# Performance work log

Measured on AMD Instinct MI355X. Metric: run time of the kernel, lower is better.

The kernel has to match this reference:

```python
import jax, jax.numpy as jnp
import numpy as np

NUM_HEADS = 16
HIDDEN = 1024
HEAD_DIM = HIDDEN // NUM_HEADS
B, S, D = 2, 2048, 1024


def setup_inputs() -> dict:
    key = jax.random.key(0)
    ks = jax.random.split(key, 7)
    scale = 1.0 / np.sqrt(D)
    return {
        "query": jax.random.normal(ks[0], (B, S, D), dtype=jnp.float32),
        "key": jax.random.normal(ks[1], (B, S, D), dtype=jnp.float32),
        "value": jax.random.normal(ks[2], (B, S, D), dtype=jnp.float32),
        "Wk_w": jax.random.normal(ks[3], (HIDDEN, D), dtype=jnp.float32) * scale,
        "Wk_b": jax.random.normal(ks[4], (HIDDEN,), dtype=jnp.float32) * scale,
        "Wv_w": jax.random.normal(ks[5], (HIDDEN, D), dtype=jnp.float32) * scale,
        "Wv_b": jax.random.normal(ks[6], (HIDDEN,), dtype=jnp.float32) * scale,
    }


def reference(query, key, value, Wk_w, Wk_b, Wv_w, Wv_b):
    # NOTE: in the original torch module, self.W_v is assigned twice, so the
    # SAME Linear (Wv) projects both key and value; Wk projects query.
    b, s, _ = query.shape

    def split_heads(x):  # [b,s,hidden] -> [b,h,s,hd]
        return x.reshape(b, s, NUM_HEADS, HEAD_DIM).transpose(0, 2, 1, 3)

    q = split_heads(query @ Wk_w.T + Wk_b)
    k = split_heads(key @ Wv_w.T + Wv_b)
    v = split_heads(value @ Wv_w.T + Wv_b)

    scores = jnp.einsum("bhqd,bhkd->bhqk", q, k) / jnp.sqrt(
        jnp.asarray(HEAD_DIM, dtype=q.dtype))
    probs = jax.nn.softmax(scores, axis=-1)
    out = jnp.einsum("bhqk,bhkd->bhqd", probs, v)
    return out.transpose(0, 2, 1, 3).reshape(b, s, NUM_HEADS * HEAD_DIM)
```

## Files before the change

kernel.cpp:

```cpp
#include <hip/hip_runtime.h>
#include <stdint.h>

typedef unsigned short u16;
typedef uint32_t u32;
typedef __bf16 bf16x8 __attribute__((ext_vector_type(8)));
typedef float f32x4 __attribute__((ext_vector_type(4)));
typedef float f32x16 __attribute__((ext_vector_type(16)));
typedef u16 u16x4 __attribute__((ext_vector_type(4)));
typedef u16 u16x8 __attribute__((ext_vector_type(8)));

#define XQ_OFF 0ul
#define XK_OFF 4194304ul
#define XV_OFF 8388608ul
#define WK_OFF 12582912ul
#define WV_OFF 13631488ul
#define Q_OFF  14680064ul
#define K_OFF  18874368ul
#define V_OFF  23068672ul

#define SCQ 0.18033688011112042f

#if __has_builtin(__builtin_amdgcn_exp2f)
#define EXP2F(x) __builtin_amdgcn_exp2f(x)
#else
#define EXP2F(x) exp2f(x)
#endif

__device__ __forceinline__ u16 f2bf(float f) {
  u32 u = __float_as_uint(f);
  u32 r = (u + 0x7fffu + ((u >> 16) & 1u)) >> 16;
  return (u16)r;
}

__device__ __forceinline__ u32 pk2(float a, float b) {
  typedef __bf16 bf2_t __attribute__((ext_vector_type(2)));
  typedef float f2_t __attribute__((ext_vector_type(2)));
  f2_t v; v[0] = a; v[1] = b;
  bf2_t h = __builtin_convertvector(v, bf2_t);
  union { bf2_t h; u32 u; } cv; cv.h = h; return cv.u;
}

__device__ __forceinline__ void load_lds16(const void* g, void* l) {
  __builtin_amdgcn_global_load_lds(
      (const __attribute__((address_space(1))) u32*)g,
      (__attribute__((address_space(3))) u32*)l, 16, 0, 0);
}

__device__ __forceinline__ u32 swz(u32 L) {
  return L ^ (((L >> 7) & 1u) << 4) ^ (((L >> 10) & 3u) << 5);
}

__global__ __launch_bounds__(256) void cvt_tile_kernel(
    const float* __restrict__ xq, const float* __restrict__ xk,
    const float* __restrict__ xv, const float* __restrict__ wk,
    const float* __restrict__ wv, u16* __restrict__ ws) {
  __shared__ u16 tile[4096];
  const int bid = blockIdx.x;
  const float* src; size_t dstbase; int rt, ktp;
  if (bid < 3072) {
    int m = bid >> 10, loc = bid & 1023;
    src = (m == 0) ? xq : (m == 1) ? xk : xv;
    dstbase = (size_t)m * 4194304ul;
    rt = loc >> 4; ktp = loc & 15;
  } else {
    int r2 = bid - 3072;
    int m = r2 >> 8, loc = r2 & 255;
    src = m ? wv : wk;
    dstbase = WK_OFF + (size_t)m * 1048576ul;
    rt = loc >> 4; ktp = loc & 15;
  }
  const int t = threadIdx.x;
  const int row0 = t >> 4, c = t & 15;
  const int k = c * 4;
  const float* s = src + (size_t)(rt * 64 + row0) * 1024ul + ktp * 64 + k;
#pragma unroll
  for (int i = 0; i < 4; ++i) {
    float4 v = *(const float4*)(s + (size_t)i * 16384ul);
    int row = row0 + i * 16;
    u32* p = (u32*)(tile + ((k >> 5) * 2048 + ((k >> 3) & 3) * 512 + row * 8 + (k & 7)));
    p[0] = pk2(v.x, v.y);
    p[1] = pk2(v.z, v.w);
  }
  __syncthreads();
  u16* dst = ws + dstbase + (size_t)(rt * 32 + ktp * 2) * 2048ul;
#pragma unroll
  for (int so = 0; so < 4096; so += 2048)
    *(u16x8*)(dst + so + t * 8) = *(const u16x8*)(tile + so + t * 8);
}

__global__ __launch_bounds__(256, 2) void proj_kernel(u16* __restrict__ ws,
                                                      const float* __restrict__ bk,
                                                      const float* __restrict__ bv) {
  const int proj = blockIdx.z;
  const int mtile = blockIdx.x;
  const int ntile = blockIdx.y;
  const u16* A = ws + (size_t)proj * 4194304ul;
  const u16* Bw = ws + ((proj == 0) ? WK_OFF : WV_OFF);
  const float* bias = (proj == 0) ? bk : bv;
  u16* outQ = ws + Q_OFF;
  u16* outK = ws + K_OFF;
  u16* outV = ws + V_OFF;

  const int t = threadIdx.x;
  const int w = t >> 6, lane = t & 63;
  const int wm = w >> 1, wn = w & 1;
  const int g = lane >> 4, c = lane & 15;

  __shared__ __align__(16) u16 smem[32768];

  const u16* Ag = A + (size_t)(2 * mtile) * 65536ul;
  const u16* Bg = Bw + (size_t)(2 * ntile) * 65536ul;
  const u32 t8 = (u32)t * 8u;
  const u32 so = swz((u32)t * 16u) >> 1;

  u32 poff[4];
#pragma unroll
  for (int mt = 0; mt < 4; ++mt)
    poff[mt] = swz((u32)((g << 10) | ((mt * 16 + c) << 4))) >> 1;

#define PSTAGE(buf, kt)                                            \
  do {                                                             \
    u16* bb = smem + (buf) * 8192;                                 \
    const size_t ko = (size_t)(kt) * 2048ul + so;                  \
    load_lds16(Ag + ko, bb + t8);                                  \
    load_lds16(Ag + 65536ul + ko, bb + 2048 + t8);                 \
    load_lds16(Bg + ko, bb + 4096 + t8);                           \
    load_lds16(Bg + 65536ul + ko, bb + 6144 + t8);                 \
  } while (0)

#define PFRAGS_MFMA(buf)                                                        \
  do {                                                                          \
    const u16* Ap = smem + (buf) * 8192 + wm * 2048;                            \
    const u16* Bp = smem + (buf) * 8192 + 4096 + wn * 2048;                     \
    bf16x8 af[4], bfv[4];                                                       \
    _Pragma("unroll") for (int mt = 0; mt < 4; ++mt)                            \
        af[mt] = *(const bf16x8*)(Ap + poff[mt]);                               \
    _Pragma("unroll") for (int nt = 0; nt < 4; ++nt)                            \
        bfv[nt] = *(const bf16x8*)(Bp + poff[nt]);                              \
    _Pragma("unroll") for (int mt = 0; mt < 4; ++mt)                            \
        _Pragma("unroll") for (int nt = 0; nt < 4; ++nt)                        \
            acc[mt][nt] = __builtin_amdgcn_mfma_f32_16x16x32_bf16(              \
                af[mt], bfv[nt], acc[mt][nt], 0, 0, 0);                         \
  } while (0)

  f32x4 acc[4][4];
#pragma unroll
  for (int mt = 0; mt < 4; ++mt)
#pragma unroll
    for (int nt = 0; nt < 4; ++nt) acc[mt][nt] = (f32x4){0.f, 0.f, 0.f, 0.f};

  PSTAGE(0, 0);
  PSTAGE(1, 1);
  PSTAGE(2, 2);
  PSTAGE(3, 3);

#pragma unroll 1
  for (int p = 0; p < 15; ++p) {
    asm volatile("s_waitcnt vmcnt(8)\n\ts_barrier" ::: "memory");
    const int b0 = (2 * p) & 3;
    PFRAGS_MFMA(b0);
    PFRAGS_MFMA(b0 + 1);
    __builtin_amdgcn_s_barrier();
    if (p < 14) {
      PSTAGE(b0, 2 * p + 4);
      PSTAGE(b0 + 1, 2 * p + 5);
    }
  }
  asm volatile("s_waitcnt vmcnt(0)\n\ts_barrier" ::: "memory");
  PFRAGS_MFMA(2);
  PFRAGS_MFMA(3);
#undef PSTAGE
#undef PFRAGS_MFMA

  const int m0 = mtile * 128 + wm * 64;
  const int n0 = ntile * 128 + wn * 64;
  if (proj == 2) {
#pragma unroll
    for (int nt = 0; nt < 4; ++nt) {
      const int col = n0 + nt * 16 + c;
      const float bvv = bias[col];
      const int h = col >> 6, d = col & 63;
#pragma unroll
      for (int mt = 0; mt < 4; ++mt) {
        const int mbase = m0 + mt * 16 + g * 4;
        const int b = mbase >> 11;
        const int bh = b * 16 + h;
        const int s = mbase & 2047;
        u16x4 pk;
#pragma unroll
        for (int r = 0; r < 4; ++r) pk[r] = f2bf(acc[mt][nt][r] + bvv);
        size_t idx = (size_t)bh * 131072ul + (size_t)(s >> 6) * 4096ul +
                     (size_t)((s & 63) >> 3) * 512ul + (size_t)d * 8ul + (size_t)(s & 7);
        *(u16x4*)(outV + idx) = pk;
      }
    }
  } else {
    __syncthreads();
    u16* Ew = smem + w * 4096;
#pragma unroll
    for (int nt = 0; nt < 4; ++nt) {
      const int d = nt * 16 + c;
      const float bvv = bias[n0 + nt * 16 + c];
#pragma unroll
      for (int mt = 0; mt < 4; ++mt) {
#pragma unroll
        for (int r = 0; r < 4; ++r) {
          const int srow = mt * 16 + g * 4 + r;
          float y = acc[mt][nt][r] + bvv;
          if (proj == 0) y *= SCQ;
          Ew[(d >> 3) * 512 + srow * 8 + (d & 7)] = f2bf(y);
        }
      }
    }
    __syncthreads();
    const int b = mtile >> 4;
    const int bh = b * 16 + ntile * 2 + wn;
    if (proj == 0) {
      u16* base = outQ + (size_t)bh * 131072ul + (size_t)(mtile & 15) * 8192ul + wm * 512;
#pragma unroll
      for (int i = 0; i < 8; ++i)
        *(u16x8*)(base + i * 1024 + lane * 8) = *(const u16x8*)(Ew + i * 512 + lane * 8);
    } else {
      u16* base = outK + (size_t)bh * 131072ul + (size_t)((mtile & 15) * 2 + wm) * 4096ul;
#pragma unroll
      for (int i = 0; i < 8; ++i)
        *(u16x8*)(base + i * 512 + lane * 8) = *(const u16x8*)(Ew + i * 512 + lane * 8);
    }
  }
}

__global__ __launch_bounds__(512, 4) void attn_kernel(u16* __restrict__ ws,
                                                      float* __restrict__ out) {
  const int bh = blockIdx.x, qtile = blockIdx.y;
  const int b = bh >> 4, h = bh & 15;
  const int t = threadIdx.x, w = t >> 6, lane = t & 63;
  const int c32 = lane & 31, g2 = lane >> 5;
  const int hf = w >> 2;
  const int wi = w & 3;

  __shared__ __align__(16) u16 smemA[32768];

  const u16* Qg = ws + Q_OFF + (size_t)bh * 131072ul + (size_t)qtile * 8192ul;

  const int hfs = t >> 8, tt = t & 255;
  const u16* KgS = ws + K_OFF + (size_t)bh * 131072ul + (size_t)hfs * 65536ul;
  const u16* VgS = ws + V_OFF + (size_t)bh * 131072ul + (size_t)hfs * 65536ul;
  u16* kb0 = smemA + hfs * 2 * 4096;
  u16* vb0 = smemA + 16384 + hfs * 2 * 4096;

  const u16* Kb0 = smemA + hf * 2 * 4096;
  const u16* Vb0 = smemA + 16384 + hf * 2 * 4096;

  bf16x8 qf[4];
#pragma unroll
  for (int ks = 0; ks < 4; ++ks)
    qf[ks] = *(const bf16x8*)(Qg + (size_t)(ks * 2 + g2) * 1024ul +
                              (size_t)(wi * 32 + c32) * 8ul);

  f32x16 O0, O1, Lacc;
#pragma unroll
  for (int i = 0; i < 16; ++i) { O0[i] = 0.f; O1[i] = 0.f; Lacc[i] = 0.f; }

#define STAGE_KV(buf, jj)                                          \
  do {                                                             \
    const u16* Kj = KgS + (size_t)(jj) * 4096ul;                   \
    const u16* Vj = VgS + (size_t)(jj) * 4096ul;                   \
    u16* kb = kb0 + (buf) * 4096;                                  \
    u16* vb = vb0 + (buf) * 4096;                                  \
    load_lds16(Kj + (size_t)tt * 8ul, kb + tt * 8);                \
    load_lds16(Kj + 2048ul + (size_t)tt * 8ul, kb + 2048 + tt * 8);\
    load_lds16(Vj + (size_t)tt * 8ul, vb + tt * 8);                \
    load_lds16(Vj + 2048ul + (size_t)tt * 8ul, vb + 2048 + tt * 8);\
  } while (0)

  STAGE_KV(0, 0);

#pragma unroll 1
  for (int j = 0; j < 16; ++j) {
    asm volatile("s_waitcnt vmcnt(0)\n\ts_barrier" ::: "memory");
    if (j < 15) STAGE_KV((j + 1) & 1, j + 1);
    const u16* Kb = Kb0 + (j & 1) * 4096;
    const u16* Vb = Vb0 + (j & 1) * 4096;

    f32x16 S0, S1;
#pragma unroll
    for (int i = 0; i < 16; ++i) { S0[i] = 0.f; S1[i] = 0.f; }
    __builtin_amdgcn_s_setprio(1);
#pragma unroll
    for (int ks = 0; ks < 4; ++ks) {
      bf16x8 kf0 = *(const bf16x8*)(Kb + (ks * 2 + g2) * 512 + c32 * 8);
      bf16x8 kf1 = *(const bf16x8*)(Kb + (ks * 2 + g2) * 512 + (32 + c32) * 8);
      S0 = __builtin_amdgcn_mfma_f32_32x32x16_bf16(kf0, qf[ks], S0, 0, 0, 0);
      S1 = __builtin_amdgcn_mfma_f32_32x32x16_bf16(kf1, qf[ks], S1, 0, 0, 0);
    }
    __builtin_amdgcn_s_setprio(0);

#pragma unroll
    for (int i = 0; i < 16; ++i) { S0[i] = EXP2F(S0[i]); S1[i] = EXP2F(S1[i]); }
    Lacc += S0;
    Lacc += S1;

    u32 pa[4][4];
#pragma unroll
    for (int half = 0; half < 2; ++half) {
      const f32x16& Sx = half ? S1 : S0;
#pragma unroll
      for (int sub = 0; sub < 2; ++sub) {
        const int rb = sub * 8;
        u32 q0 = pk2(Sx[rb + 0], Sx[rb + 1]);
        u32 q1 = pk2(Sx[rb + 2], Sx[rb + 3]);
        u32 q2 = pk2(Sx[rb + 4], Sx[rb + 5]);
        u32 q3 = pk2(Sx[rb + 6], Sx[rb + 7]);
        asm volatile("v_permlane32_swap_b32 %0, %1" : "+v"(q0), "+v"(q2));
        asm volatile("v_permlane32_swap_b32 %0, %1" : "+v"(q1), "+v"(q3));
        const int kstep = half * 2 + sub;
        pa[kstep][0] = q0; pa[kstep][1] = q1; pa[kstep][2] = q2; pa[kstep][3] = q3;
      }
    }

    __builtin_amdgcn_s_setprio(1);
#pragma unroll
    for (int kstep = 0; kstep < 4; ++kstep) {
      union { u32 u[4]; bf16x8 b; } pcv;
#pragma unroll
      for (int i = 0; i < 4; ++i) pcv.u[i] = pa[kstep][i];
      bf16x8 vf0 = *(const bf16x8*)(Vb + (kstep * 2 + g2) * 512 + c32 * 8);
      bf16x8 vf1 = *(const bf16x8*)(Vb + (kstep * 2 + g2) * 512 + (32 + c32) * 8);
      O0 = __builtin_amdgcn_mfma_f32_32x32x16_bf16(pcv.b, vf0, O0, 0, 0, 0);
      O1 = __builtin_amdgcn_mfma_f32_32x32x16_bf16(pcv.b, vf1, O1, 0, 0, 0);
    }
    __builtin_amdgcn_s_setprio(0);
  }
#undef STAGE_KV

  float lp = 0.f;
#pragma unroll
  for (int i = 0; i < 16; ++i) lp += Lacc[i];
  float lA = lp, lB = lp;
  asm volatile("v_permlane32_swap_b32 %0, %1" : "+v"(lA), "+v"(lB));
  float Ltot = lA + lB;

  asm volatile("s_waitcnt lgkmcnt(0)" ::: "memory");
  __syncthreads();
  float* exch = (float*)smemA;
  float* ex = exch + (size_t)(wi * 64 + lane) * 33ul;
  if (hf == 1) {
#pragma unroll
    for (int i = 0; i < 16; ++i) { ex[i] = O0[i]; ex[16 + i] = O1[i]; }
    ex[32] = Ltot;
  }
  __syncthreads();
  if (hf == 0) {
    const float Ltc = Ltot + ex[32];
    const int q0 = qtile * 128 + wi * 32;
    float* outb = out + (size_t)(b * 2048 + q0) * 1024ul + h * 64 + c32;
#pragma unroll
    for (int r = 0; r < 16; ++r) {
      const int qr = (r & 3) + 8 * (r >> 2) + 4 * g2;
      int lv = __builtin_amdgcn_ds_bpermute(qr << 2, __float_as_int(Ltc));
      const float inv = 1.0f / __int_as_float(lv);
      float* rp = outb + (size_t)qr * 1024ul;
      rp[0] = (O0[r] + ex[r]) * inv;
      rp[32] = (O1[r] + ex[16 + r]) * inv;
    }
  }
}

extern "C" void kernel_launch(void* const* d_in, const int* in_sizes, int n_in,
                              void* d_out, int out_size, void* d_ws, size_t ws_size,
                              hipStream_t stream) {
  const float* q = (const float*)d_in[0];
  const float* k = (const float*)d_in[1];
  const float* v = (const float*)d_in[2];
  const float* wk = (const float*)d_in[3];
  const float* bk = (const float*)d_in[4];
  const float* wv = (const float*)d_in[5];
  const float* bv = (const float*)d_in[6];
  u16* ws = (u16*)d_ws;
  float* out = (float*)d_out;

  cvt_tile_kernel<<<3584, 256, 0, stream>>>(q, k, v, wk, wv, ws);
  proj_kernel<<<dim3(32, 8, 3), 256, 0, stream>>>(ws, bk, bv);
  attn_kernel<<<dim3(32, 16), 512, 0, stream>>>(ws, out);
}
```

Measured before the change: 174.6 us.

## Fuse fp32-to-bf16 conversion into projection GEMM, dropping separate convert kernel

New measurement: 197.0 us. 1.13x slower.

```diff
diff --git a/kernel.cpp b/kernel.cpp
--- a/kernel.cpp
+++ b/kernel.cpp
@@ -9,11 +9,6 @@
 typedef u16 u16x4 __attribute__((ext_vector_type(4)));
 typedef u16 u16x8 __attribute__((ext_vector_type(8)));
 
-#define XQ_OFF 0ul
-#define XK_OFF 4194304ul
-#define XV_OFF 8388608ul
-#define WK_OFF 12582912ul
-#define WV_OFF 13631488ul
 #define Q_OFF  14680064ul
 #define K_OFF  18874368ul
 #define V_OFF  23068672ul
@@ -46,56 +41,16 @@
       (__attribute__((address_space(3))) u32*)l, 16, 0, 0);
 }
 
-__device__ __forceinline__ u32 swz(u32 L) {
-  return L ^ (((L >> 7) & 1u) << 4) ^ (((L >> 10) & 3u) << 5);
-}
-
-__global__ __launch_bounds__(256) void cvt_tile_kernel(
+__global__ __launch_bounds__(256, 2) void proj_kernel(
     const float* __restrict__ xq, const float* __restrict__ xk,
     const float* __restrict__ xv, const float* __restrict__ wk,
-    const float* __restrict__ wv, u16* __restrict__ ws) {
-  __shared__ u16 tile[4096];
-  const int bid = blockIdx.x;
-  const float* src; size_t dstbase; int rt, ktp;
-  if (bid < 3072) {
-    int m = bid >> 10, loc = bid & 1023;
-    src = (m == 0) ? xq : (m == 1) ? xk : xv;
-    dstbase = (size_t)m * 4194304ul;
-    rt = loc >> 4; ktp = loc & 15;
-  } else {
-    int r2 = bid - 3072;
-    int m = r2 >> 8, loc = r2 & 255;
-    src = m ? wv : wk;
-    dstbase = WK_OFF + (size_t)m * 1048576ul;
-    rt = loc >> 4; ktp = loc & 15;
-  }
-  const int t = threadIdx.x;
-  const int row0 = t >> 4, c = t & 15;
-  const int k = c * 4;
-  const float* s = src + (size_t)(rt * 64 + row0) * 1024ul + ktp * 64 + k;
-#pragma unroll
-  for (int i = 0; i < 4; ++i) {
-    float4 v = *(const float4*)(s + (size_t)i * 16384ul);
-    int row = row0 + i * 16;
-    u32* p = (u32*)(tile + ((k >> 5) * 2048 + ((k >> 3) & 3) * 512 + row * 8 + (k & 7)));
-    p[0] = pk2(v.x, v.y);
-    p[1] = pk2(v.z, v.w);
-  }
-  __syncthreads();
-  u16* dst = ws + dstbase + (size_t)(rt * 32 + ktp * 2) * 2048ul;
-#pragma unroll
-  for (int so = 0; so < 4096; so += 2048)
-    *(u16x8*)(dst + so + t * 8) = *(const u16x8*)(tile + so + t * 8);
-}
-
-__global__ __launch_bounds__(256, 2) void proj_kernel(u16* __restrict__ ws,
-                                                      const float* __restrict__ bk,
-                                                      const float* __restrict__ bv) {
+    const float* __restrict__ wv, const float* __restrict__ bk,
+    const float* __restrict__ bv, u16* __restrict__ ws) {
   const int proj = blockIdx.z;
   const int mtile = blockIdx.x;
   const int ntile = blockIdx.y;
-  const u16* A = ws + (size_t)proj * 4194304ul;
-  const u16* Bw = ws + ((proj == 0) ? WK_OFF : WV_OFF);
+  const float* xa = (proj == 0) ? xq : (proj == 1) ? xk : xv;
+  const float* wsrc = (proj == 0) ? wk : wv;
   const float* bias = (proj == 0) ? bk : bv;
   u16* outQ = ws + Q_OFF;
   u16* outK = ws + K_OFF;
@@ -106,71 +61,72 @@
   const int wm = w >> 1, wn = w & 1;
   const int g = lane >> 4, c = lane & 15;
 
-  __shared__ __align__(16) u16 smem[32768];
-
-  const u16* Ag = A + (size_t)(2 * mtile) * 65536ul;
-  const u16* Bg = Bw + (size_t)(2 * ntile) * 65536ul;
-  const u32 t8 = (u32)t * 8u;
-  const u32 so = swz((u32)t * 16u) >> 1;
-
-  u32 poff[4];
+  __shared__ __align__(16) float smemf[16384];
+
+  const int srow = t >> 3;
+  const int lchunk = (t & 7) ^ (srow & 7);
+  const float* As0 = xa + (size_t)(mtile * 128 + srow) * 1024ul + lchunk * 4;
+  const float* Bs0 = wsrc + (size_t)(ntile * 128 + srow) * 1024ul + lchunk * 4;
+
+#define PSTAGE(buf, kt)                                                      \
+  do {                                                                       \
+    float* ab = smemf + (buf) * 8192 + t * 4;                                \
+    float* bb = smemf + (buf) * 8192 + 4096 + t * 4;                         \
+    const float* as = As0 + (size_t)(kt) * 32ul;                             \
+    const float* bs = Bs0 + (size_t)(kt) * 32ul;                             \
+    load_lds16(as, ab);                                                      \
+    load_lds16(as + 32768, ab + 1024);                                       \
+    load_lds16(as + 65536, ab + 2048);                                       \
+    load_lds16(as + 98304, ab + 3072);                                       \
+    load_lds16(bs, bb);                                                      \
+    load_lds16(bs + 32768, bb + 1024);                                       \
+    load_lds16(bs + 65536, bb + 2048);                                       \
+    load_lds16(bs + 98304, bb + 3072);                                       \
+  } while (0)
+
+#define PFRAG(Reg, r)                                                        \
+  ({                                                                         \
+    const float* rp_ = (Reg) + (r) * 32;                                     \
+    f32x4 v0_ = *(const f32x4*)(rp_ + (((g * 2) ^ ((r) & 7)) << 2));         \
+    f32x4 v1_ = *(const f32x4*)(rp_ + (((g * 2 + 1) ^ ((r) & 7)) << 2));     \
+    union { u32 u[4]; bf16x8 b; } cvu_;                                      \
+    cvu_.u[0] = pk2(v0_[0], v0_[1]); cvu_.u[1] = pk2(v0_[2], v0_[3]);        \
+    cvu_.u[2] = pk2(v1_[0], v1_[1]); cvu_.u[3] = pk2(v1_[2], v1_[3]);        \
+    cvu_.b;                                                                  \
+  })
+
+#define PCOMPUTE(buf)                                                        \
+  do {                                                                       \
+    const float* Ar = smemf + (buf) * 8192;                                  \
+    const float* Br = smemf + (buf) * 8192 + 4096;                           \
+    bf16x8 af[4], bfv[4];                                                    \
+    _Pragma("unroll") for (int mt = 0; mt < 4; ++mt)                         \
+        af[mt] = PFRAG(Ar, wm * 64 + mt * 16 + c);                           \
+    _Pragma("unroll") for (int nt = 0; nt < 4; ++nt)                         \
+        bfv[nt] = PFRAG(Br, wn * 64 + nt * 16 + c);                          \
+    _Pragma("unroll") for (int mt = 0; mt < 4; ++mt)                         \
+      _Pragma("unroll") for (int nt = 0; nt < 4; ++nt)                       \
+          acc[mt][nt] = __builtin_amdgcn_mfma_f32_16x16x32_bf16(             \
+              af[mt], bfv[nt], acc[mt][nt], 0, 0, 0);                        \
+  } while (0)
+
+  f32x4 acc[4][4];
 #pragma unroll
   for (int mt = 0; mt < 4; ++mt)
-    poff[mt] = swz((u32)((g << 10) | ((mt * 16 + c) << 4))) >> 1;
-
-#define PSTAGE(buf, kt)                                            \
-  do {                                                             \
-    u16* bb = smem + (buf) * 8192;                                 \
-    const size_t ko = (size_t)(kt) * 2048ul + so;                  \
-    load_lds16(Ag + ko, bb + t8);                                  \
-    load_lds16(Ag + 65536ul + ko, bb + 2048 + t8);                 \
-    load_lds16(Bg + ko, bb + 4096 + t8);                           \
-    load_lds16(Bg + 65536ul + ko, bb + 6144 + t8);                 \
-  } while (0)
-
-#define PFRAGS_MFMA(buf)                                                        \
-  do {                                                                          \
-    const u16* Ap = smem + (buf) * 8192 + wm * 2048;                            \
-    const u16* Bp = smem + (buf) * 8192 + 4096 + wn * 2048;                     \
-    bf16x8 af[4], bfv[4];                                                       \
-    _Pragma("unroll") for (int mt = 0; mt < 4; ++mt)                            \
-        af[mt] = *(const bf16x8*)(Ap + poff[mt]);                               \
-    _Pragma("unroll") for (int nt = 0; nt < 4; ++nt)                            \
-        bfv[nt] = *(const bf16x8*)(Bp + poff[nt]);                              \
-    _Pragma("unroll") for (int mt = 0; mt < 4; ++mt)                            \
-        _Pragma("unroll") for (int nt = 0; nt < 4; ++nt)                        \
-            acc[mt][nt] = __builtin_amdgcn_mfma_f32_16x16x32_bf16(              \
-                af[mt], bfv[nt], acc[mt][nt], 0, 0, 0);                         \
-  } while (0)
-
-  f32x4 acc[4][4];
-#pragma unroll
-  for (int mt = 0; mt < 4; ++mt)
 #pragma unroll
     for (int nt = 0; nt < 4; ++nt) acc[mt][nt] = (f32x4){0.f, 0.f, 0.f, 0.f};
 
   PSTAGE(0, 0);
-  PSTAGE(1, 1);
-  PSTAGE(2, 2);
-  PSTAGE(3, 3);
 
 #pragma unroll 1
-  for (int p = 0; p < 15; ++p) {
-    asm volatile("s_waitcnt vmcnt(8)\n\ts_barrier" ::: "memory");
-    const int b0 = (2 * p) & 3;
-    PFRAGS_MFMA(b0);
-    PFRAGS_MFMA(b0 + 1);
-    __builtin_amdgcn_s_barrier();
-    if (p < 14) {
-      PSTAGE(b0, 2 * p + 4);
-      PSTAGE(b0 + 1, 2 * p + 5);
-    }
-  }
-  asm volatile("s_waitcnt vmcnt(0)\n\ts_barrier" ::: "memory");
-  PFRAGS_MFMA(2);
-  PFRAGS_MFMA(3);
+  for (int kt = 0; kt < 32; ++kt) {
+    asm volatile("s_waitcnt vmcnt(0)\n\ts_barrier" ::: "memory");
+    if (kt < 31) PSTAGE((kt + 1) & 1, kt + 1);
+    PCOMPUTE(kt & 1);
+  }
 #undef PSTAGE
-#undef PFRAGS_MFMA
+#undef PFRAG
+#undef PCOMPUTE
 
   const int m0 = mtile * 128 + wm * 64;
   const int n0 = ntile * 128 + wn * 64;
@@ -196,6 +152,7 @@
     }
   } else {
     __syncthreads();
+    u16* smem = (u16*)smemf;
     u16* Ew = smem + w * 4096;
 #pragma unroll
     for (int nt = 0; nt < 4; ++nt) {
@@ -205,10 +162,10 @@
       for (int mt = 0; mt < 4; ++mt) {
 #pragma unroll
         for (int r = 0; r < 4; ++r) {
-          const int srow = mt * 16 + g * 4 + r;
+          const int srow2 = mt * 16 + g * 4 + r;
           float y = acc[mt][nt][r] + bvv;
           if (proj == 0) y *= SCQ;
-          Ew[(d >> 3) * 512 + srow * 8 + (d & 7)] = f2bf(y);
+          Ew[(d >> 3) * 512 + srow2 * 8 + (d & 7)] = f2bf(y);
         }
       }
     }
@@ -379,7 +336,6 @@
   u16* ws = (u16*)d_ws;
   float* out = (float*)d_out;
 
-  cvt_tile_kernel<<<3584, 256, 0, stream>>>(q, k, v, wk, wv, ws);
-  proj_kernel<<<dim3(32, 8, 3), 256, 0, stream>>>(ws, bk, bv);
+  proj_kernel<<<dim3(32, 8, 3), 256, 0, stream>>>(q, k, v, wk, wv, bk, bv, ws);
   attn_kernel<<<dim3(32, 16), 512, 0, stream>>>(ws, out);
 }
```
